# Optimization experiments

Hardware: AMD Instinct MI355X
Metric: run time of the kernel (lower is better)

Reference implementation:

```python
import jax, jax.numpy as jnp
import numpy as np

R, C, N, E, H, F, ED, G, L = 1, 4, 50000, 200000, 128, 128, 16, 64, 2


def setup_inputs() -> dict:
    key = jax.random.key(0)
    ks = jax.random.split(key, 16)
    s = 0.05
    return {
        "x": jax.random.normal(ks[0], (R * C * N, H), jnp.float32),
        "batch": jnp.sort(jax.random.randint(ks[1], (N,), 0, G)),
        "edge_index": jax.random.randint(ks[2], (2, E), 0, N),
        "edge_attr": jax.random.normal(ks[3], (1, 1, E, ED), jnp.float32),
        "node_mask": jax.random.uniform(ks[4], (R, C, N, 1), jnp.float32),
        "edge_mask": jax.random.uniform(ks[5], (R, C, E, 1), jnp.float32),
        "W_be": jax.random.normal(ks[6], (ED, H), jnp.float32) * s,
        "b_be": jnp.zeros((H,), jnp.float32),
        "eps": jnp.zeros((L,), jnp.float32),
        "W1": jax.random.normal(ks[7], (L, H, H), jnp.float32) * s,
        "b1": jnp.zeros((L, H), jnp.float32),
        "W2": jax.random.normal(ks[8], (L, H, H), jnp.float32) * s,
        "b2": jnp.zeros((L, H), jnp.float32),
        "Wm1": jax.random.normal(ks[9], (H, H), jnp.float32) * s,
        "bm1": jnp.zeros((H,), jnp.float32),
        "Wm2": jax.random.normal(ks[10], (H, F), jnp.float32) * s,
        "bm2": jnp.zeros((F,), jnp.float32),
    }


def reference(x, batch, edge_index, edge_attr, node_mask, edge_mask,
              W_be, b_be, eps, W1, b1, W2, b2, Wm1, bm1, Wm2, bm2):
    gelu = lambda v: jax.nn.gelu(v, approximate=False)  # torch F.gelu default is erf
    src, dst = edge_index[0], edge_index[1]
    # bond encoder, shared across conv layers: (1,1,E,H)
    ee = edge_attr @ W_be + b_be
    for l in range(L):
        ux = x.reshape(R, C, N, H)
        # gather + add + GELU + edge-weight multiply: (R,C,E,H)
        msg = gelu(ux[:, :, src, :] + ee) * edge_mask
        # scatter_sum over edges into destination nodes
        agg = jnp.zeros_like(ux).at[:, :, dst, :].add(msg)
        h = (1.0 + eps[l]) * x + agg.reshape(x.shape)
        # conv MLP: Linear -> GELU -> Linear, then outer GELU (norm=Identity, dropout=0)
        h = gelu(h @ W1[l] + b1[l]) @ W2[l] + b2[l]
        x = gelu(h)
    # final node MLP (PyG MLP, norm=None): Linear -> GELU -> Linear
    x = gelu(x @ Wm1 + bm1) @ Wm2 + bm2  # (R*C*N, F)
    x4 = x.reshape(R, C, N, F)
    # masked mean-pool per (repeat, centroid, graph)
    num = jnp.zeros((R, C, G, F), x.dtype).at[:, :, batch, :].add(x4 * node_mask)
    den = jnp.zeros((R, C, G, 1), x.dtype).at[:, :, batch, :].add(node_mask) + 1e-7
    pooled = (num / den).transpose(0, 2, 1, 3).reshape(-1, F)  # (R*G*C, F)
    return pooled
```

## Files before the change

### kernel.cpp

```cpp
#include <hip/hip_runtime.h>
#include <math.h>

#define NN 50000
#define EN 200000
#define CC 4
#define HH 128
#define GG 64
#define LDSA 136
#define LDSF 132

typedef __attribute__((ext_vector_type(8))) short bs8;
typedef __attribute__((ext_vector_type(4))) float f32x4;

__device__ __forceinline__ unsigned short f2bf(float f) {
  unsigned int u = __float_as_uint(f);
  u += 0x7FFFu + ((u >> 16) & 1u);
  return (unsigned short)(u >> 16);
}
__device__ __forceinline__ float bf2f(unsigned short h) {
  return __uint_as_float(((unsigned int)h) << 16);
}
__device__ __forceinline__ float gelu_f(float x) {
  float z = fabsf(x) * 0.7071067811865476f;
  float t = __builtin_amdgcn_rcpf(fmaf(0.3275911f, z, 1.0f));
  float poly = t * fmaf(t, fmaf(t, fmaf(t, fmaf(t, 1.061405429f, -1.453152027f),
                                        1.421413741f), -0.284496736f), 0.254829592f);
  float e = fmaf(-poly, __expf(-z * z), 1.0f);
  return 0.5f * x * (1.0f + copysignf(e, x));
}

__global__ __launch_bounds__(256) void count_kernel(const int* __restrict__ dst,
                                                    int* __restrict__ counts) {
  int e = blockIdx.x * 256 + threadIdx.x;
  if (e < EN) atomicAdd(&counts[dst[e]], 1);
}

__global__ __launch_bounds__(256) void block_sum_kernel(const int* __restrict__ counts,
                                                        int* __restrict__ bsums) {
  int tid = threadIdx.x;
  int i = blockIdx.x * 256 + tid;
  int v = (i < NN) ? counts[i] : 0;
#pragma unroll
  for (int d = 1; d < 64; d <<= 1) v += __shfl_xor(v, d);
  __shared__ int ws4[4];
  if ((tid & 63) == 0) ws4[tid >> 6] = v;
  __syncthreads();
  if (tid == 0) bsums[blockIdx.x] = ws4[0] + ws4[1] + ws4[2] + ws4[3];
}

__global__ __launch_bounds__(256) void bsum_scan_kernel(const int* __restrict__ bsums,
                                                        int* __restrict__ boffs, int nb) {
  int tid = threadIdx.x, lane = tid & 63, wv = tid >> 6;
  int v = (tid < nb) ? bsums[tid] : 0;
  int s = v;
#pragma unroll
  for (int d = 1; d < 64; d <<= 1) { int t = __shfl_up(s, d); if (lane >= d) s += t; }
  __shared__ int wsum[4];
  if (lane == 63) wsum[wv] = s;
  __syncthreads();
  int pre = 0;
  for (int j = 0; j < wv; ++j) pre += wsum[j];
  if (tid < nb) boffs[tid] = pre + s - v;
}

__global__ __launch_bounds__(256) void block_scan_kernel(const int* __restrict__ counts,
                                                         const int* __restrict__ boffs,
                                                         int* __restrict__ offsets,
                                                         int* __restrict__ cursor) {
  int tid = threadIdx.x, lane = tid & 63, wv = tid >> 6;
  int i = blockIdx.x * 256 + tid;
  int v = (i < NN) ? counts[i] : 0;
  int s = v;
#pragma unroll
  for (int d = 1; d < 64; d <<= 1) { int t = __shfl_up(s, d); if (lane >= d) s += t; }
  __shared__ int wsum[4];
  if (lane == 63) wsum[wv] = s;
  __syncthreads();
  int pre = boffs[blockIdx.x];
  for (int j = 0; j < wv; ++j) pre += wsum[j];
  if (i < NN) { int e = pre + s - v; offsets[i] = e; cursor[i] = e; }
  if (i == 0) offsets[NN] = EN;
}

__global__ __launch_bounds__(256) void fill_kernel(const int* __restrict__ dst,
                                                   int* __restrict__ cursor,
                                                   int* __restrict__ csr_e) {
  int e = blockIdx.x * 256 + threadIdx.x;
  if (e < EN) {
    int pos = atomicAdd(&cursor[dst[e]], 1);
    csr_e[pos] = e;
  }
}

__global__ __launch_bounds__(256) void prep_w_kernel(const float* __restrict__ W1,
                                                     const float* __restrict__ W2,
                                                     const float* __restrict__ Wm1,
                                                     const float* __restrict__ Wm2,
                                                     unsigned short* __restrict__ wts) {
  int m = blockIdx.x >> 6;
  int idx = (blockIdx.x & 63) * 256 + threadIdx.x;
  const float* src = (m == 0) ? W1 : (m == 1) ? W1 + 16384 : (m == 2) ? W2
                     : (m == 3) ? W2 + 16384 : (m == 4) ? Wm1 : Wm2;
  unsigned short* dhi = wts + m * 32768;
  unsigned short* dlo = dhi + 16384;
  int n = idx >> 7, k = idx & 127;
  float v = src[k * HH + n];
  unsigned short hi = f2bf(v);
  dhi[n * HH + k] = hi;
  dlo[n * HH + k] = f2bf(v - bf2f(hi));
}

__global__ __launch_bounds__(256) void ee_kernel(const float* __restrict__ eattr,
                                                 const float* __restrict__ Wbe,
                                                 const float* __restrict__ bbe,
                                                 float* __restrict__ ee) {
  __shared__ float Ws[16 * HH];
  __shared__ float Ea[16 * 16];
  int tid = threadIdx.x;
  int e0 = blockIdx.x * 16;
#pragma unroll
  for (int i = 0; i < 8; ++i) Ws[tid + i * 256] = Wbe[tid + i * 256];
  Ea[tid] = eattr[(size_t)e0 * 16 + tid];
  __syncthreads();
  int h = tid & 127, half = tid >> 7;
  float bb = bbe[h];
#pragma unroll
  for (int j = 0; j < 8; ++j) {
    int el = j * 2 + half;
    float acc = bb;
#pragma unroll
    for (int d = 0; d < 16; ++d) acc += Ea[el * 16 + d] * Ws[d * HH + h];
    ee[(size_t)(e0 + el) * HH + h] = acc;
  }
}

__global__ __launch_bounds__(256) void agg_kernel(const float* __restrict__ x,
                                                  const float* __restrict__ ee,
                                                  const float* __restrict__ emask,
                                                  const int* __restrict__ src,
                                                  const int* __restrict__ off,
                                                  const int* __restrict__ csr_e,
                                                  const float* __restrict__ epsp, int layer,
                                                  float* __restrict__ hout) {
  int wv = threadIdx.x >> 6, lane = threadIdx.x & 63;
  int v = blockIdx.x * 4 + wv;
  int h2 = lane * 2;
  float2 acc[CC];
#pragma unroll
  for (int c = 0; c < CC; ++c) { acc[c].x = 0.f; acc[c].y = 0.f; }
  int beg = off[v], end = off[v + 1];
  int e = 0, s = 0;
  if (beg < end) { e = csr_e[beg]; s = src[e]; }
  for (int t = beg; t < end; ++t) {
    int tn = t + 1;
    int e2 = 0, s2 = 0;
    if (tn < end) { e2 = csr_e[tn]; s2 = src[e2]; }
    float2 ev = *(const float2*)(ee + (size_t)e * HH + h2);
#pragma unroll
    for (int c = 0; c < CC; ++c) {
      float em = emask[c * EN + e];
      float2 xv = *(const float2*)(x + (size_t)(c * NN + s) * HH + h2);
      acc[c].x += gelu_f(xv.x + ev.x) * em;
      acc[c].y += gelu_f(xv.y + ev.y) * em;
    }
    e = e2; s = s2;
  }
  float ep = 1.0f + epsp[layer];
#pragma unroll
  for (int c = 0; c < CC; ++c) {
    float2 xs = *(const float2*)(x + (size_t)(c * NN + v) * HH + h2);
    float2 o;
    o.x = ep * xs.x + acc[c].x;
    o.y = ep * xs.y + acc[c].y;
    *(float2*)(hout + (size_t)(c * NN + v) * HH + h2) = o;
  }
}

__global__ __launch_bounds__(256, 2) void mlp_kernel(
    const float* __restrict__ in,
    const unsigned short* __restrict__ w1hi, const unsigned short* __restrict__ w1lo,
    const float* __restrict__ b1,
    const unsigned short* __restrict__ w2hi, const unsigned short* __restrict__ w2lo,
    const float* __restrict__ b2,
    float* __restrict__ out,
    const float* __restrict__ nmask, const int* __restrict__ batch,
    float* __restrict__ num, int mode) {
  __shared__ __align__(16) unsigned short AB[128 * LDSA];
  __shared__ int kk[64];
  unsigned short* Ahi = AB;
  unsigned short* Alo = AB + 64 * LDSA;
  int tid = threadIdx.x;
  int row0 = blockIdx.x * 64;
  int lane = tid & 63, wq = tid >> 6;
  int ln = lane & 15, quad = lane >> 4;

  bs8 b1h[4][2], b1l[4][2];
#pragma unroll
  for (int ks = 0; ks < 4; ++ks)
#pragma unroll
    for (int nt = 0; nt < 2; ++nt) {
      int wrow = ((wq * 2 + nt) * 16 + ln) * HH + ks * 32 + quad * 8;
      b1h[ks][nt] = *(const bs8*)(w1hi + wrow);
      b1l[ks][nt] = *(const bs8*)(w1lo + wrow);
    }

#pragma unroll
  for (int i = 0; i < 8; ++i) {
    int idx = tid + i * 256;
    int r = idx >> 5, c4 = idx & 31;
    float4 vv = *(const float4*)(in + (size_t)(row0 + r) * HH + c4 * 4);
    unsigned short h0 = f2bf(vv.x), h1 = f2bf(vv.y), h2 = f2bf(vv.z), h3 = f2bf(vv.w);
    ushort4 hv; hv.x = h0; hv.y = h1; hv.z = h2; hv.w = h3;
    ushort4 lv;
    lv.x = f2bf(vv.x - bf2f(h0)); lv.y = f2bf(vv.y - bf2f(h1));
    lv.z = f2bf(vv.z - bf2f(h2)); lv.w = f2bf(vv.w - bf2f(h3));
    *(ushort4*)(Ahi + r * LDSA + c4 * 4) = hv;
    *(ushort4*)(Alo + r * LDSA + c4 * 4) = lv;
  }
  __syncthreads();

  f32x4 acc[4][2];
#pragma unroll
  for (int mt = 0; mt < 4; ++mt)
#pragma unroll
    for (int nt = 0; nt < 2; ++nt)
#pragma unroll
      for (int r = 0; r < 4; ++r) acc[mt][nt][r] = 0.f;
#pragma unroll
  for (int ks = 0; ks < 4; ++ks) {
    bs8 ah[4], al[4];
#pragma unroll
    for (int mt = 0; mt < 4; ++mt) {
      ah[mt] = *(const bs8*)(Ahi + (mt * 16 + ln) * LDSA + ks * 32 + quad * 8);
      al[mt] = *(const bs8*)(Alo + (mt * 16 + ln) * LDSA + ks * 32 + quad * 8);
    }
#pragma unroll
    for (int nt = 0; nt < 2; ++nt)
#pragma unroll
      for (int mt = 0; mt < 4; ++mt) {
        acc[mt][nt] = __builtin_amdgcn_mfma_f32_16x16x32_bf16(al[mt], b1h[ks][nt], acc[mt][nt], 0, 0, 0);
        acc[mt][nt] = __builtin_amdgcn_mfma_f32_16x16x32_bf16(ah[mt], b1l[ks][nt], acc[mt][nt], 0, 0, 0);
        acc[mt][nt] = __builtin_amdgcn_mfma_f32_16x16x32_bf16(ah[mt], b1h[ks][nt], acc[mt][nt], 0, 0, 0);
      }
  }
  __syncthreads();

  bs8 b2h[4][2], b2l[4][2];
#pragma unroll
  for (int ks = 0; ks < 4; ++ks)
#pragma unroll
    for (int nt = 0; nt < 2; ++nt) {
      int wrow = ((wq * 2 + nt) * 16 + ln) * HH + ks * 32 + quad * 8;
      b2h[ks][nt] = *(const bs8*)(w2hi + wrow);
      b2l[ks][nt] = *(const bs8*)(w2lo + wrow);
    }

#pragma unroll
  for (int nt = 0; nt < 2; ++nt) {
    int col = (wq * 2 + nt) * 16 + ln;
    float bb = b1[col];
#pragma unroll
    for (int mt = 0; mt < 4; ++mt)
#pragma unroll
      for (int r = 0; r < 4; ++r) {
        float tv = gelu_f(acc[mt][nt][r] + bb);
        unsigned short th = f2bf(tv);
        int rr = mt * 16 + quad * 4 + r;
        Ahi[rr * LDSA + col] = th;
        Alo[rr * LDSA + col] = f2bf(tv - bf2f(th));
      }
  }
  __syncthreads();

#pragma unroll
  for (int mt = 0; mt < 4; ++mt)
#pragma unroll
    for (int nt = 0; nt < 2; ++nt)
#pragma unroll
      for (int r = 0; r < 4; ++r) acc[mt][nt][r] = 0.f;
  if (mode == 0) {
#pragma unroll
    for (int ks = 0; ks < 4; ++ks) {
      bs8 ah[4], al[4];
#pragma unroll
      for (int mt = 0; mt < 4; ++mt) {
        ah[mt] = *(const bs8*)(Ahi + (mt * 16 + ln) * LDSA + ks * 32 + quad * 8);
        al[mt] = *(const bs8*)(Alo + (mt * 16 + ln) * LDSA + ks * 32 + quad * 8);
      }
#pragma unroll
      for (int nt = 0; nt < 2; ++nt)
#pragma unroll
        for (int mt = 0; mt < 4; ++mt) {
          acc[mt][nt] = __builtin_amdgcn_mfma_f32_16x16x32_bf16(al[mt], b2h[ks][nt], acc[mt][nt], 0, 0, 0);
          acc[mt][nt] = __builtin_amdgcn_mfma_f32_16x16x32_bf16(ah[mt], b2l[ks][nt], acc[mt][nt], 0, 0, 0);
          acc[mt][nt] = __builtin_amdgcn_mfma_f32_16x16x32_bf16(ah[mt], b2h[ks][nt], acc[mt][nt], 0, 0, 0);
        }
    }
#pragma unroll
    for (int nt = 0; nt < 2; ++nt) {
      int col = (wq * 2 + nt) * 16 + ln;
      float bb = b2[col];
#pragma unroll
      for (int mt = 0; mt < 4; ++mt)
#pragma unroll
        for (int r = 0; r < 4; ++r) {
          float o = gelu_f(acc[mt][nt][r] + bb);
          out[(size_t)(row0 + mt * 16 + quad * 4 + r) * HH + col] = o;
        }
    }
  } else {
#pragma unroll
    for (int ks = 0; ks < 4; ++ks) {
      bs8 ah[4], al[4];
#pragma unroll
      for (int mt = 0; mt < 4; ++mt) {
        ah[mt] = *(const bs8*)(Ahi + (mt * 16 + ln) * LDSA + ks * 32 + quad * 8);
        al[mt] = *(const bs8*)(Alo + (mt * 16 + ln) * LDSA + ks * 32 + quad * 8);
      }
#pragma unroll
      for (int nt = 0; nt < 2; ++nt)
#pragma unroll
        for (int mt = 0; mt < 4; ++mt) {
          acc[mt][nt] = __builtin_amdgcn_mfma_f32_16x16x32_bf16(al[mt], b2h[ks][nt], acc[mt][nt], 0, 0, 0);
          acc[mt][nt] = __builtin_amdgcn_mfma_f32_16x16x32_bf16(ah[mt], b2l[ks][nt], acc[mt][nt], 0, 0, 0);
          acc[mt][nt] = __builtin_amdgcn_mfma_f32_16x16x32_bf16(ah[mt], b2h[ks][nt], acc[mt][nt], 0, 0, 0);
        }
    }
    __syncthreads();
    float* Tf = (float*)AB;
#pragma unroll
    for (int nt = 0; nt < 2; ++nt) {
      int col = (wq * 2 + nt) * 16 + ln;
      float bb = b2[col];
#pragma unroll
      for (int mt = 0; mt < 4; ++mt)
#pragma unroll
        for (int r = 0; r < 4; ++r) {
          int rl = mt * 16 + quad * 4 + r;
          int gr = row0 + rl;
          Tf[rl * LDSF + col] = (acc[mt][nt][r] + bb) * nmask[gr];
        }
    }
    if (tid < 64) {
      int gr = row0 + tid;
      int c = gr / NN;
      int n = gr - c * NN;
      kk[tid] = (c << 6) | batch[n];
    }
    __syncthreads();
    if (tid < 128) {
      int col = tid;
      float a2 = 0.f;
      int cur = kk[0];
      for (int r = 0; r < 64; ++r) {
        int k2 = kk[r];
        if (k2 != cur) {
          atomicAdd(&num[((size_t)(cur & 63) * CC + (cur >> 6)) * HH + col], a2);
          a2 = 0.f;
          cur = k2;
        }
        a2 += Tf[r * LDSF + col];
      }
      atomicAdd(&num[((size_t)(cur & 63) * CC + (cur >> 6)) * HH + col], a2);
    }
  }
}

__global__ __launch_bounds__(256) void pool_finalize_kernel(const float* __restrict__ num,
                                                            const int* __restrict__ batch,
                                                            const float* __restrict__ nmask,
                                                            float* __restrict__ outp) {
  int g = blockIdx.x >> 2, c = blockIdx.x & 3;
  int lo = 0, hi = NN;
  while (lo < hi) { int m = (lo + hi) >> 1; if (batch[m] < g) lo = m + 1; else hi = m; }
  int start = lo;
  hi = NN;
  while (lo < hi) { int m = (lo + hi) >> 1; if (batch[m] < g + 1) lo = m + 1; else hi = m; }
  int end = lo;
  int tid = threadIdx.x;
  float d = 0.f;
  for (int n = start + tid; n < end; n += 256) d += nmask[c * NN + n];
#pragma unroll
  for (int k = 1; k < 64; k <<= 1) d += __shfl_xor(d, k);
  __shared__ float ws4[4];
  if ((tid & 63) == 0) ws4[tid >> 6] = d;
  __syncthreads();
  float den = ws4[0] + ws4[1] + ws4[2] + ws4[3] + 1e-7f;
  if (tid < 128) {
    int idx = blockIdx.x * 128 + tid;
    outp[idx] = num[idx] / den;
  }
}

extern "C" void kernel_launch(void* const* d_in, const int* in_sizes, int n_in,
                              void* d_out, int out_size, void* d_ws, size_t ws_size,
                              hipStream_t stream) {
  const float* x_in  = (const float*)d_in[0];
  const int*   batch = (const int*)d_in[1];
  const int*   eidx  = (const int*)d_in[2];
  const float* eattr = (const float*)d_in[3];
  const float* nmask = (const float*)d_in[4];
  const float* emask = (const float*)d_in[5];
  const float* Wbe   = (const float*)d_in[6];
  const float* bbe   = (const float*)d_in[7];
  const float* epsp  = (const float*)d_in[8];
  const float* W1    = (const float*)d_in[9];
  const float* b1    = (const float*)d_in[10];
  const float* W2    = (const float*)d_in[11];
  const float* b2    = (const float*)d_in[12];
  const float* Wm1   = (const float*)d_in[13];
  const float* bm1   = (const float*)d_in[14];
  const float* Wm2   = (const float*)d_in[15];
  const float* bm2   = (const float*)d_in[16];
  float* outp = (float*)d_out;

  const int* srcp = eidx;
  const int* dstp = eidx + EN;

  char* ws = (char*)d_ws;
  float* ee   = (float*)(ws);
  float* hbuf = (float*)(ws + 102400000);
  float* xbuf = (float*)(ws + 204800000);
  int* counts  = (int*)(ws + 307200000);
  int* offsets = counts + NN;
  int* cursor  = offsets + NN + 1;
  int* csr_e   = cursor + NN;
  unsigned short* wts = (unsigned short*)(ws + 307200000 + 1400016);
  int* bsums = (int*)ws;
  int* boffs = (int*)(ws + 1024);
  float* num = (float*)ws;

  const int NB = (NN + 255) / 256;

  hipMemsetAsync(counts, 0, NN * sizeof(int), stream);
  count_kernel<<<(EN + 255) / 256, 256, 0, stream>>>(dstp, counts);
  block_sum_kernel<<<NB, 256, 0, stream>>>(counts, bsums);
  bsum_scan_kernel<<<1, 256, 0, stream>>>(bsums, boffs, NB);
  block_scan_kernel<<<NB, 256, 0, stream>>>(counts, boffs, offsets, cursor);
  fill_kernel<<<(EN + 255) / 256, 256, 0, stream>>>(dstp, cursor, csr_e);

  prep_w_kernel<<<384, 256, 0, stream>>>(W1, W2, Wm1, Wm2, wts);

  ee_kernel<<<EN / 16, 256, 0, stream>>>(eattr, Wbe, bbe, ee);

  agg_kernel<<<NN / 4, 256, 0, stream>>>(x_in, ee, emask, srcp, offsets, csr_e, epsp, 0, hbuf);
  mlp_kernel<<<(CC * NN) / 64, 256, 0, stream>>>(hbuf, wts + 0, wts + 16384, b1,
                                                 wts + 65536, wts + 81920, b2,
                                                 xbuf, nmask, batch, num, 0);
  agg_kernel<<<NN / 4, 256, 0, stream>>>(xbuf, ee, emask, srcp, offsets, csr_e, epsp, 1, hbuf);
  mlp_kernel<<<(CC * NN) / 64, 256, 0, stream>>>(hbuf, wts + 32768, wts + 49152, b1 + 128,
                                                 wts + 98304, wts + 114688, b2 + 128,
                                                 xbuf, nmask, batch, num, 0);
  hipMemsetAsync(num, 0, 131072, stream);
  mlp_kernel<<<(CC * NN) / 64, 256, 0, stream>>>(xbuf, wts + 131072, wts + 147456, bm1,
                                                 wts + 163840, wts + 180224, bm2,
                                                 (float*)nullptr, nmask, batch, num, 1);
  pool_finalize_kernel<<<GG * CC, 256, 0, stream>>>(num, batch, nmask, outp);
}
```

Baseline: 770.9 us.

## Fuse edge aggregation into per-layer MLP kernel with node-major activation layout

Merges the gather/GELU/scatter aggregation and the two-linear MLP into one layer kernel. Each block aggregates 16 nodes across all 4 centroids, with half-waves splitting edges and combining through shuffles, and writes the result straight into LDS as bf16 hi/lo tiles, so the fp32 hbuf round trip to global memory is gone. Intermediate activations move to a node-major (node, centroid) layout, so one gathered source node reads 4 contiguous rows, and the final MLP+pool kernel is adapted to that layout. The cost is that edge-gather latency now sits inside an MFMA kernel limited to 2 blocks per CU, and per-node degree imbalance stalls the whole block.

```diff
diff --git a/kernel.cpp b/kernel.cpp
--- a/kernel.cpp
+++ b/kernel.cpp
@@ -134,65 +134,28 @@
   }
 }
 
-__global__ __launch_bounds__(256) void agg_kernel(const float* __restrict__ x,
-                                                  const float* __restrict__ ee,
-                                                  const float* __restrict__ emask,
-                                                  const int* __restrict__ src,
-                                                  const int* __restrict__ off,
-                                                  const int* __restrict__ csr_e,
-                                                  const float* __restrict__ epsp, int layer,
-                                                  float* __restrict__ hout) {
-  int wv = threadIdx.x >> 6, lane = threadIdx.x & 63;
-  int v = blockIdx.x * 4 + wv;
-  int h2 = lane * 2;
-  float2 acc[CC];
-#pragma unroll
-  for (int c = 0; c < CC; ++c) { acc[c].x = 0.f; acc[c].y = 0.f; }
-  int beg = off[v], end = off[v + 1];
-  int e = 0, s = 0;
-  if (beg < end) { e = csr_e[beg]; s = src[e]; }
-  for (int t = beg; t < end; ++t) {
-    int tn = t + 1;
-    int e2 = 0, s2 = 0;
-    if (tn < end) { e2 = csr_e[tn]; s2 = src[e2]; }
-    float2 ev = *(const float2*)(ee + (size_t)e * HH + h2);
-#pragma unroll
-    for (int c = 0; c < CC; ++c) {
-      float em = emask[c * EN + e];
-      float2 xv = *(const float2*)(x + (size_t)(c * NN + s) * HH + h2);
-      acc[c].x += gelu_f(xv.x + ev.x) * em;
-      acc[c].y += gelu_f(xv.y + ev.y) * em;
-    }
-    e = e2; s = s2;
-  }
-  float ep = 1.0f + epsp[layer];
-#pragma unroll
-  for (int c = 0; c < CC; ++c) {
-    float2 xs = *(const float2*)(x + (size_t)(c * NN + v) * HH + h2);
-    float2 o;
-    o.x = ep * xs.x + acc[c].x;
-    o.y = ep * xs.y + acc[c].y;
-    *(float2*)(hout + (size_t)(c * NN + v) * HH + h2) = o;
-  }
-}
-
-__global__ __launch_bounds__(256, 2) void mlp_kernel(
-    const float* __restrict__ in,
+__global__ __launch_bounds__(256, 2) void layer_kernel(
+    const float* __restrict__ x, const float* __restrict__ ee,
+    const float* __restrict__ emask,
+    const int* __restrict__ src, const int* __restrict__ off,
+    const int* __restrict__ csr_e,
+    const float* __restrict__ epsp, int layer,
     const unsigned short* __restrict__ w1hi, const unsigned short* __restrict__ w1lo,
     const float* __restrict__ b1,
     const unsigned short* __restrict__ w2hi, const unsigned short* __restrict__ w2lo,
     const float* __restrict__ b2,
-    float* __restrict__ out,
-    const float* __restrict__ nmask, const int* __restrict__ batch,
-    float* __restrict__ num, int mode) {
+    float* __restrict__ out) {
   __shared__ __align__(16) unsigned short AB[128 * LDSA];
-  __shared__ int kk[64];
   unsigned short* Ahi = AB;
   unsigned short* Alo = AB + 64 * LDSA;
   int tid = threadIdx.x;
+  int lane = tid & 63, wv = tid >> 6;
+  int node0 = blockIdx.x * 16;
   int row0 = blockIdx.x * 64;
-  int lane = tid & 63, wq = tid >> 6;
+  int half = lane >> 5, l32 = lane & 31;
+  int c4 = l32 * 4;
   int ln = lane & 15, quad = lane >> 4;
+  int wq = wv;
 
   bs8 b1h[4][2], b1l[4][2];
 #pragma unroll
@@ -204,18 +167,59 @@
       b1l[ks][nt] = *(const bs8*)(w1lo + wrow);
     }
 
-#pragma unroll
-  for (int i = 0; i < 8; ++i) {
-    int idx = tid + i * 256;
-    int r = idx >> 5, c4 = idx & 31;
-    float4 vv = *(const float4*)(in + (size_t)(row0 + r) * HH + c4 * 4);
-    unsigned short h0 = f2bf(vv.x), h1 = f2bf(vv.y), h2 = f2bf(vv.z), h3 = f2bf(vv.w);
-    ushort4 hv; hv.x = h0; hv.y = h1; hv.z = h2; hv.w = h3;
-    ushort4 lv;
-    lv.x = f2bf(vv.x - bf2f(h0)); lv.y = f2bf(vv.y - bf2f(h1));
-    lv.z = f2bf(vv.z - bf2f(h2)); lv.w = f2bf(vv.w - bf2f(h3));
-    *(ushort4*)(Ahi + r * LDSA + c4 * 4) = hv;
-    *(ushort4*)(Alo + r * LDSA + c4 * 4) = lv;
+  float ep = 1.0f + epsp[layer];
+#pragma unroll
+  for (int j = 0; j < 4; ++j) {
+    int v = node0 + wv * 4 + j;
+    float4 acc[CC];
+#pragma unroll
+    for (int c = 0; c < CC; ++c) { acc[c].x = 0.f; acc[c].y = 0.f; acc[c].z = 0.f; acc[c].w = 0.f; }
+    int beg = off[v], end = off[v + 1];
+    int t0 = beg + half;
+    int e = 0, s = 0;
+    if (t0 < end) { e = csr_e[t0]; s = src[e]; }
+    for (int t = t0; t < end; t += 2) {
+      int tn = t + 2;
+      int e2 = 0, s2 = 0;
+      if (tn < end) { e2 = csr_e[tn]; s2 = src[e2]; }
+      float4 ev = *(const float4*)(ee + (size_t)e * HH + c4);
+#pragma unroll
+      for (int c = 0; c < CC; ++c) {
+        float em = emask[c * EN + e];
+        size_t xrow = (layer == 0) ? ((size_t)c * NN + s) : ((size_t)s * CC + c);
+        float4 xv = *(const float4*)(x + xrow * HH + c4);
+        acc[c].x += gelu_f(xv.x + ev.x) * em;
+        acc[c].y += gelu_f(xv.y + ev.y) * em;
+        acc[c].z += gelu_f(xv.z + ev.z) * em;
+        acc[c].w += gelu_f(xv.w + ev.w) * em;
+      }
+      e = e2; s = s2;
+    }
+#pragma unroll
+    for (int c = 0; c < CC; ++c) {
+      acc[c].x += __shfl_xor(acc[c].x, 32);
+      acc[c].y += __shfl_xor(acc[c].y, 32);
+      acc[c].z += __shfl_xor(acc[c].z, 32);
+      acc[c].w += __shfl_xor(acc[c].w, 32);
+    }
+#pragma unroll
+    for (int cc = 0; cc < 2; ++cc) {
+      int c = half * 2 + cc;
+      size_t srow = (layer == 0) ? ((size_t)c * NN + v) : ((size_t)v * CC + c);
+      float4 xs = *(const float4*)(x + srow * HH + c4);
+      float ox = fmaf(ep, xs.x, acc[c].x);
+      float oy = fmaf(ep, xs.y, acc[c].y);
+      float oz = fmaf(ep, xs.z, acc[c].z);
+      float ow = fmaf(ep, xs.w, acc[c].w);
+      unsigned short h0 = f2bf(ox), h1 = f2bf(oy), h2 = f2bf(oz), h3 = f2bf(ow);
+      ushort4 hv; hv.x = h0; hv.y = h1; hv.z = h2; hv.w = h3;
+      ushort4 lv;
+      lv.x = f2bf(ox - bf2f(h0)); lv.y = f2bf(oy - bf2f(h1));
+      lv.z = f2bf(oz - bf2f(h2)); lv.w = f2bf(ow - bf2f(h3));
+      int rl = (wv * 4 + j) * 4 + c;
+      *(ushort4*)(Ahi + rl * LDSA + c4) = hv;
+      *(ushort4*)(Alo + rl * LDSA + c4) = lv;
+    }
   }
   __syncthreads();
 
@@ -278,90 +282,187 @@
     for (int nt = 0; nt < 2; ++nt)
 #pragma unroll
       for (int r = 0; r < 4; ++r) acc[mt][nt][r] = 0.f;
-  if (mode == 0) {
-#pragma unroll
-    for (int ks = 0; ks < 4; ++ks) {
-      bs8 ah[4], al[4];
+#pragma unroll
+  for (int ks = 0; ks < 4; ++ks) {
+    bs8 ah[4], al[4];
+#pragma unroll
+    for (int mt = 0; mt < 4; ++mt) {
+      ah[mt] = *(const bs8*)(Ahi + (mt * 16 + ln) * LDSA + ks * 32 + quad * 8);
+      al[mt] = *(const bs8*)(Alo + (mt * 16 + ln) * LDSA + ks * 32 + quad * 8);
+    }
+#pragma unroll
+    for (int nt = 0; nt < 2; ++nt)
 #pragma unroll
       for (int mt = 0; mt < 4; ++mt) {
-        ah[mt] = *(const bs8*)(Ahi + (mt * 16 + ln) * LDSA + ks * 32 + quad * 8);
-        al[mt] = *(const bs8*)(Alo + (mt * 16 + ln) * LDSA + ks * 32 + quad * 8);
-      }
-#pragma unroll
-      for (int nt = 0; nt < 2; ++nt)
-#pragma unroll
-        for (int mt = 0; mt < 4; ++mt) {
-          acc[mt][nt] = __builtin_amdgcn_mfma_f32_16x16x32_bf16(al[mt], b2h[ks][nt], acc[mt][nt], 0, 0, 0);
-          acc[mt][nt] = __builtin_amdgcn_mfma_f32_16x16x32_bf16(ah[mt], b2l[ks][nt], acc[mt][nt], 0, 0, 0);
-          acc[mt][nt] = __builtin_amdgcn_mfma_f32_16x16x32_bf16(ah[mt], b2h[ks][nt], acc[mt][nt], 0, 0, 0);
-        }
-    }
+        acc[mt][nt] = __builtin_amdgcn_mfma_f32_16x16x32_bf16(al[mt], b2h[ks][nt], acc[mt][nt], 0, 0, 0);
+        acc[mt][nt] = __builtin_amdgcn_mfma_f32_16x16x32_bf16(ah[mt], b2l[ks][nt], acc[mt][nt], 0, 0, 0);
+        acc[mt][nt] = __builtin_amdgcn_mfma_f32_16x16x32_bf16(ah[mt], b2h[ks][nt], acc[mt][nt], 0, 0, 0);
+      }
+  }
+#pragma unroll
+  for (int nt = 0; nt < 2; ++nt) {
+    int col = (wq * 2 + nt) * 16 + ln;
+    float bb = b2[col];
+#pragma unroll
+    for (int mt = 0; mt < 4; ++mt)
+#pragma unroll
+      for (int r = 0; r < 4; ++r) {
+        float o = gelu_f(acc[mt][nt][r] + bb);
+        out[(size_t)(row0 + mt * 16 + quad * 4 + r) * HH + col] = o;
+      }
+  }
+}
+
+__global__ __launch_bounds__(256, 2) void mlp_pool_kernel(
+    const float* __restrict__ in,
+    const unsigned short* __restrict__ w1hi, const unsigned short* __restrict__ w1lo,
+    const float* __restrict__ b1,
+    const unsigned short* __restrict__ w2hi, const unsigned short* __restrict__ w2lo,
+    const float* __restrict__ b2,
+    const float* __restrict__ nmask, const int* __restrict__ batch,
+    float* __restrict__ num) {
+  __shared__ __align__(16) unsigned short AB[128 * LDSA];
+  __shared__ int kk[16];
+  unsigned short* Ahi = AB;
+  unsigned short* Alo = AB + 64 * LDSA;
+  int tid = threadIdx.x;
+  int row0 = blockIdx.x * 64;
+  int node0 = row0 >> 2;
+  int lane = tid & 63, wq = tid >> 6;
+  int ln = lane & 15, quad = lane >> 4;
+
+  bs8 b1h[4][2], b1l[4][2];
+#pragma unroll
+  for (int ks = 0; ks < 4; ++ks)
 #pragma unroll
     for (int nt = 0; nt < 2; ++nt) {
-      int col = (wq * 2 + nt) * 16 + ln;
-      float bb = b2[col];
-#pragma unroll
-      for (int mt = 0; mt < 4; ++mt)
-#pragma unroll
-        for (int r = 0; r < 4; ++r) {
-          float o = gelu_f(acc[mt][nt][r] + bb);
-          out[(size_t)(row0 + mt * 16 + quad * 4 + r) * HH + col] = o;
-        }
-    }
-  } else {
-#pragma unroll
-    for (int ks = 0; ks < 4; ++ks) {
-      bs8 ah[4], al[4];
+      int wrow = ((wq * 2 + nt) * 16 + ln) * HH + ks * 32 + quad * 8;
+      b1h[ks][nt] = *(const bs8*)(w1hi + wrow);
+      b1l[ks][nt] = *(const bs8*)(w1lo + wrow);
+    }
+#pragma unroll
+  for (int i = 0; i < 8; ++i) {
+    int idx = tid + i * 256;
+    int r = idx >> 5, cc4 = idx & 31;
+    float4 vv = *(const float4*)(in + (size_t)(row0 + r) * HH + cc4 * 4);
+    unsigned short h0 = f2bf(vv.x), h1 = f2bf(vv.y), h2 = f2bf(vv.z), h3 = f2bf(vv.w);
+    ushort4 hv; hv.x = h0; hv.y = h1; hv.z = h2; hv.w = h3;
+    ushort4 lv;
+    lv.x = f2bf(vv.x - bf2f(h0)); lv.y = f2bf(vv.y - bf2f(h1));
+    lv.z = f2bf(vv.z - bf2f(h2)); lv.w = f2bf(vv.w - bf2f(h3));
+    *(ushort4*)(Ahi + r * LDSA + cc4 * 4) = hv;
+    *(ushort4*)(Alo + r * LDSA + cc4 * 4) = lv;
+  }
+  if (tid < 16) kk[tid] = batch[node0 + tid];
+  __syncthreads();
+
+  f32x4 acc[4][2];
+#pragma unroll
+  for (int mt = 0; mt < 4; ++mt)
+#pragma unroll
+    for (int nt = 0; nt < 2; ++nt)
+#pragma unroll
+      for (int r = 0; r < 4; ++r) acc[mt][nt][r] = 0.f;
+#pragma unroll
+  for (int ks = 0; ks < 4; ++ks) {
+    bs8 ah[4], al[4];
+#pragma unroll
+    for (int mt = 0; mt < 4; ++mt) {
+      ah[mt] = *(const bs8*)(Ahi + (mt * 16 + ln) * LDSA + ks * 32 + quad * 8);
+      al[mt] = *(const bs8*)(Alo + (mt * 16 + ln) * LDSA + ks * 32 + quad * 8);
+    }
+#pragma unroll
+    for (int nt = 0; nt < 2; ++nt)
 #pragma unroll
       for (int mt = 0; mt < 4; ++mt) {
-        ah[mt] = *(const bs8*)(Ahi + (mt * 16 + ln) * LDSA + ks * 32 + quad * 8);
-        al[mt] = *(const bs8*)(Alo + (mt * 16 + ln) * LDSA + ks * 32 + quad * 8);
-      }
-#pragma unroll
-      for (int nt = 0; nt < 2; ++nt)
-#pragma unroll
-        for (int mt = 0; mt < 4; ++mt) {
-          acc[mt][nt] = __builtin_amdgcn_mfma_f32_16x16x32_bf16(al[mt], b2h[ks][nt], acc[mt][nt], 0, 0, 0);
-          acc[mt][nt] = __builtin_amdgcn_mfma_f32_16x16x32_bf16(ah[mt], b2l[ks][nt], acc[mt][nt], 0, 0, 0);
-          acc[mt][nt] = __builtin_amdgcn_mfma_f32_16x16x32_bf16(ah[mt], b2h[ks][nt], acc[mt][nt], 0, 0, 0);
-        }
-    }
-    __syncthreads();
-    float* Tf = (float*)AB;
+        acc[mt][nt] = __builtin_amdgcn_mfma_f32_16x16x32_bf16(al[mt], b1h[ks][nt], acc[mt][nt], 0, 0, 0);
+        acc[mt][nt] = __builtin_amdgcn_mfma_f32_16x16x32_bf16(ah[mt], b1l[ks][nt], acc[mt][nt], 0, 0, 0);
+        acc[mt][nt] = __builtin_amdgcn_mfma_f32_16x16x32_bf16(ah[mt], b1h[ks][nt], acc[mt][nt], 0, 0, 0);
+      }
+  }
+  __syncthreads();
+
+  bs8 b2h[4][2], b2l[4][2];
+#pragma unroll
+  for (int ks = 0; ks < 4; ++ks)
 #pragma unroll
     for (int nt = 0; nt < 2; ++nt) {
-      int col = (wq * 2 + nt) * 16 + ln;
-      float bb = b2[col];
-#pragma unroll
-      for (int mt = 0; mt < 4; ++mt)
-#pragma unroll
-        for (int r = 0; r < 4; ++r) {
-          int rl = mt * 16 + quad * 4 + r;
-          int gr = row0 + rl;
-          Tf[rl * LDSF + col] = (acc[mt][nt][r] + bb) * nmask[gr];
-        }
-    }
-    if (tid < 64) {
-      int gr = row0 + tid;
-      int c = gr / NN;
-      int n = gr - c * NN;
-      kk[tid] = (c << 6) | batch[n];
-    }
-    __syncthreads();
-    if (tid < 128) {
-      int col = tid;
+      int wrow = ((wq * 2 + nt) * 16 + ln) * HH + ks * 32 + quad * 8;
+      b2h[ks][nt] = *(const bs8*)(w2hi + wrow);
+      b2l[ks][nt] = *(const bs8*)(w2lo + wrow);
+    }
+#pragma unroll
+  for (int nt = 0; nt < 2; ++nt) {
+    int col = (wq * 2 + nt) * 16 + ln;
+    float bb = b1[col];
+#pragma unroll
+    for (int mt = 0; mt < 4; ++mt)
+#pragma unroll
+      for (int r = 0; r < 4; ++r) {
+        float tv = gelu_f(acc[mt][nt][r] + bb);
+        unsigned short th = f2bf(tv);
+        int rr = mt * 16 + quad * 4 + r;
+        Ahi[rr * LDSA + col] = th;
+        Alo[rr * LDSA + col] = f2bf(tv - bf2f(th));
+      }
+  }
+  __syncthreads();
+
+#pragma unroll
+  for (int mt = 0; mt < 4; ++mt)
+#pragma unroll
+    for (int nt = 0; nt < 2; ++nt)
+#pragma unroll
+      for (int r = 0; r < 4; ++r) acc[mt][nt][r] = 0.f;
+#pragma unroll
+  for (int ks = 0; ks < 4; ++ks) {
+    bs8 ah[4], al[4];
+#pragma unroll
+    for (int mt = 0; mt < 4; ++mt) {
+      ah[mt] = *(const bs8*)(Ahi + (mt * 16 + ln) * LDSA + ks * 32 + quad * 8);
+      al[mt] = *(const bs8*)(Alo + (mt * 16 + ln) * LDSA + ks * 32 + quad * 8);
+    }
+#pragma unroll
+    for (int nt = 0; nt < 2; ++nt)
+#pragma unroll
+      for (int mt = 0; mt < 4; ++mt) {
+        acc[mt][nt] = __builtin_amdgcn_mfma_f32_16x16x32_bf16(al[mt], b2h[ks][nt], acc[mt][nt], 0, 0, 0);
+        acc[mt][nt] = __builtin_amdgcn_mfma_f32_16x16x32_bf16(ah[mt], b2l[ks][nt], acc[mt][nt], 0, 0, 0);
+        acc[mt][nt] = __builtin_amdgcn_mfma_f32_16x16x32_bf16(ah[mt], b2h[ks][nt], acc[mt][nt], 0, 0, 0);
+      }
+  }
+  __syncthreads();
+  float* Tf = (float*)AB;
+#pragma unroll
+  for (int nt = 0; nt < 2; ++nt) {
+    int col = (wq * 2 + nt) * 16 + ln;
+    float bb = b2[col];
+#pragma unroll
+    for (int mt = 0; mt < 4; ++mt)
+#pragma unroll
+      for (int r = 0; r < 4; ++r) {
+        int rl = mt * 16 + quad * 4 + r;
+        int n = node0 + (rl >> 2), c = rl & 3;
+        Tf[rl * LDSF + col] = (acc[mt][nt][r] + bb) * nmask[c * NN + n];
+      }
+  }
+  __syncthreads();
+  if (tid < 128) {
+    int col = tid;
+#pragma unroll
+    for (int c = 0; c < 4; ++c) {
       float a2 = 0.f;
       int cur = kk[0];
-      for (int r = 0; r < 64; ++r) {
-        int k2 = kk[r];
-        if (k2 != cur) {
-          atomicAdd(&num[((size_t)(cur & 63) * CC + (cur >> 6)) * HH + col], a2);
+      for (int nl = 0; nl < 16; ++nl) {
+        int g2 = kk[nl];
+        if (g2 != cur) {
+          atomicAdd(&num[((size_t)cur * CC + c) * HH + col], a2);
           a2 = 0.f;
-          cur = k2;
+          cur = g2;
         }
-        a2 += Tf[r * LDSF + col];
-      }
-      atomicAdd(&num[((size_t)(cur & 63) * CC + (cur >> 6)) * HH + col], a2);
+        a2 += Tf[(nl * 4 + c) * LDSF + col];
+      }
+      atomicAdd(&num[((size_t)cur * CC + c) * HH + col], a2);
     }
   }
 }
@@ -418,9 +519,9 @@
   const int* dstp = eidx + EN;
 
   char* ws = (char*)d_ws;
-  float* ee   = (float*)(ws);
-  float* hbuf = (float*)(ws + 102400000);
-  float* xbuf = (float*)(ws + 204800000);
+  float* ee = (float*)(ws);
+  float* x2 = (float*)(ws + 102400000);
+  float* x1 = (float*)(ws + 204800000);
   int* counts  = (int*)(ws + 307200000);
   int* offsets = counts + NN;
   int* cursor  = offsets + NN + 1;
@@ -443,17 +544,15 @@
 
   ee_kernel<<<EN / 16, 256, 0, stream>>>(eattr, Wbe, bbe, ee);
 
-  agg_kernel<<<NN / 4, 256, 0, stream>>>(x_in, ee, emask, srcp, offsets, csr_e, epsp, 0, hbuf);
-  mlp_kernel<<<(CC * NN) / 64, 256, 0, stream>>>(hbuf, wts + 0, wts + 16384, b1,
-                                                 wts + 65536, wts + 81920, b2,
-                                                 xbuf, nmask, batch, num, 0);
-  agg_kernel<<<NN / 4, 256, 0, stream>>>(xbuf, ee, emask, srcp, offsets, csr_e, epsp, 1, hbuf);
-  mlp_kernel<<<(CC * NN) / 64, 256, 0, stream>>>(hbuf, wts + 32768, wts + 49152, b1 + 128,
-                                                 wts + 98304, wts + 114688, b2 + 128,
-                                                 xbuf, nmask, batch, num, 0);
+  layer_kernel<<<NN / 16, 256, 0, stream>>>(x_in, ee, emask, srcp, offsets, csr_e, epsp, 0,
+                                            wts + 0, wts + 16384, b1,
+                                            wts + 65536, wts + 81920, b2, x1);
+  layer_kernel<<<NN / 16, 256, 0, stream>>>(x1, ee, emask, srcp, offsets, csr_e, epsp, 1,
+                                            wts + 32768, wts + 49152, b1 + 128,
+                                            wts + 98304, wts + 114688, b2 + 128, x2);
   hipMemsetAsync(num, 0, 131072, stream);
-  mlp_kernel<<<(CC * NN) / 64, 256, 0, stream>>>(xbuf, wts + 131072, wts + 147456, bm1,
-                                                 wts + 163840, wts + 180224, bm2,
-                                                 (float*)nullptr, nmask, batch, num, 1);
+  mlp_pool_kernel<<<(CC * NN) / 64, 256, 0, stream>>>(x2, wts + 131072, wts + 147456, bm1,
+                                                      wts + 163840, wts + 180224, bm2,
+                                                      nmask, batch, num);
   pool_finalize_kernel<<<GG * CC, 256, 0, stream>>>(num, batch, nmask, outp);
 }
```

Result: slower. 900.1 us (+16.8%).

## Split edge loop across half-waves in agg and use per-wave MLP kernel

Applied to the files above, without the earlier changes.

The aggregation kernel now has each half-wave process alternate edges using float4 loads, then combines the partial sums with a cross-half shuffle. Each half writes two of the four channel outputs. The layer MLPs use a new kernel where each wave owns 16 rows and keeps its A fragments in registers. Weights are streamed from global memory or cache instead of being held in registers, LDS is used only for the per-wave intermediate, and block barriers are removed. This trades more weight loads per MFMA for higher occupancy (3 blocks) and no syncthreads, and the pooling MLP is split into its own kernel.

```diff
diff --git a/kernel.cpp b/kernel.cpp
--- a/kernel.cpp
+++ b/kernel.cpp
@@ -144,47 +144,154 @@
                                                   float* __restrict__ hout) {
   int wv = threadIdx.x >> 6, lane = threadIdx.x & 63;
   int v = blockIdx.x * 4 + wv;
-  int h2 = lane * 2;
-  float2 acc[CC];
-#pragma unroll
-  for (int c = 0; c < CC; ++c) { acc[c].x = 0.f; acc[c].y = 0.f; }
+  int half = lane >> 5, l32 = lane & 31;
+  int c4 = l32 * 4;
+  float4 acc[CC];
+#pragma unroll
+  for (int c = 0; c < CC; ++c) { acc[c].x = 0.f; acc[c].y = 0.f; acc[c].z = 0.f; acc[c].w = 0.f; }
   int beg = off[v], end = off[v + 1];
+  int t0 = beg + half;
   int e = 0, s = 0;
-  if (beg < end) { e = csr_e[beg]; s = src[e]; }
-  for (int t = beg; t < end; ++t) {
-    int tn = t + 1;
+  if (t0 < end) { e = csr_e[t0]; s = src[e]; }
+  for (int t = t0; t < end; t += 2) {
+    int tn = t + 2;
     int e2 = 0, s2 = 0;
     if (tn < end) { e2 = csr_e[tn]; s2 = src[e2]; }
-    float2 ev = *(const float2*)(ee + (size_t)e * HH + h2);
+    float4 ev = *(const float4*)(ee + (size_t)e * HH + c4);
 #pragma unroll
     for (int c = 0; c < CC; ++c) {
       float em = emask[c * EN + e];
-      float2 xv = *(const float2*)(x + (size_t)(c * NN + s) * HH + h2);
+      float4 xv = *(const float4*)(x + ((size_t)c * NN + s) * HH + c4);
       acc[c].x += gelu_f(xv.x + ev.x) * em;
       acc[c].y += gelu_f(xv.y + ev.y) * em;
+      acc[c].z += gelu_f(xv.z + ev.z) * em;
+      acc[c].w += gelu_f(xv.w + ev.w) * em;
     }
     e = e2; s = s2;
   }
+#pragma unroll
+  for (int c = 0; c < CC; ++c) {
+    acc[c].x += __shfl_xor(acc[c].x, 32);
+    acc[c].y += __shfl_xor(acc[c].y, 32);
+    acc[c].z += __shfl_xor(acc[c].z, 32);
+    acc[c].w += __shfl_xor(acc[c].w, 32);
+  }
   float ep = 1.0f + epsp[layer];
 #pragma unroll
-  for (int c = 0; c < CC; ++c) {
-    float2 xs = *(const float2*)(x + (size_t)(c * NN + v) * HH + h2);
-    float2 o;
-    o.x = ep * xs.x + acc[c].x;
-    o.y = ep * xs.y + acc[c].y;
-    *(float2*)(hout + (size_t)(c * NN + v) * HH + h2) = o;
-  }
-}
-
-__global__ __launch_bounds__(256, 2) void mlp_kernel(
+  for (int cc = 0; cc < 2; ++cc) {
+    int c = half * 2 + cc;
+    float4 xs = *(const float4*)(x + ((size_t)c * NN + v) * HH + c4);
+    float4 o;
+    o.x = fmaf(ep, xs.x, acc[c].x);
+    o.y = fmaf(ep, xs.y, acc[c].y);
+    o.z = fmaf(ep, xs.z, acc[c].z);
+    o.w = fmaf(ep, xs.w, acc[c].w);
+    *(float4*)(hout + ((size_t)c * NN + v) * HH + c4) = o;
+  }
+}
+
+__global__ __launch_bounds__(256, 3) void mlp_fast_kernel(
     const float* __restrict__ in,
     const unsigned short* __restrict__ w1hi, const unsigned short* __restrict__ w1lo,
     const float* __restrict__ b1,
     const unsigned short* __restrict__ w2hi, const unsigned short* __restrict__ w2lo,
     const float* __restrict__ b2,
-    float* __restrict__ out,
+    float* __restrict__ out) {
+  __shared__ __align__(16) unsigned short T[4][2][16 * LDSA];
+  int tid = threadIdx.x;
+  int lane = tid & 63, wv = tid >> 6;
+  int ln = lane & 15, quad = lane >> 4;
+  int row0 = blockIdx.x * 64 + wv * 16;
+  unsigned short* Thi = &T[wv][0][0];
+  unsigned short* Tlo = &T[wv][1][0];
+
+  bs8 ahi[4], alo[4];
+#pragma unroll
+  for (int ks = 0; ks < 4; ++ks) {
+    const float* p = in + (size_t)(row0 + ln) * HH + ks * 32 + quad * 8;
+    float4 v0 = *(const float4*)p;
+    float4 v1 = *(const float4*)(p + 4);
+    bs8 h, l;
+    h[0] = f2bf(v0.x); h[1] = f2bf(v0.y); h[2] = f2bf(v0.z); h[3] = f2bf(v0.w);
+    h[4] = f2bf(v1.x); h[5] = f2bf(v1.y); h[6] = f2bf(v1.z); h[7] = f2bf(v1.w);
+    l[0] = f2bf(v0.x - bf2f(h[0])); l[1] = f2bf(v0.y - bf2f(h[1]));
+    l[2] = f2bf(v0.z - bf2f(h[2])); l[3] = f2bf(v0.w - bf2f(h[3]));
+    l[4] = f2bf(v1.x - bf2f(h[4])); l[5] = f2bf(v1.y - bf2f(h[5]));
+    l[6] = f2bf(v1.z - bf2f(h[6])); l[7] = f2bf(v1.w - bf2f(h[7]));
+    ahi[ks] = h; alo[ks] = l;
+  }
+
+  f32x4 acc[8];
+#pragma unroll
+  for (int nt = 0; nt < 8; ++nt)
+#pragma unroll
+    for (int r = 0; r < 4; ++r) acc[nt][r] = 0.f;
+#pragma unroll
+  for (int nt = 0; nt < 8; ++nt)
+#pragma unroll
+    for (int ks = 0; ks < 4; ++ks) {
+      int wrow = (nt * 16 + ln) * HH + ks * 32 + quad * 8;
+      bs8 bh = *(const bs8*)(w1hi + wrow);
+      bs8 bl = *(const bs8*)(w1lo + wrow);
+      acc[nt] = __builtin_amdgcn_mfma_f32_16x16x32_bf16(alo[ks], bh, acc[nt], 0, 0, 0);
+      acc[nt] = __builtin_amdgcn_mfma_f32_16x16x32_bf16(ahi[ks], bl, acc[nt], 0, 0, 0);
+      acc[nt] = __builtin_amdgcn_mfma_f32_16x16x32_bf16(ahi[ks], bh, acc[nt], 0, 0, 0);
+    }
+
+#pragma unroll
+  for (int nt = 0; nt < 8; ++nt) {
+    int col = nt * 16 + ln;
+    float bb = b1[col];
+#pragma unroll
+    for (int r = 0; r < 4; ++r) {
+      float tv = gelu_f(acc[nt][r] + bb);
+      unsigned short th = f2bf(tv);
+      int rr = quad * 4 + r;
+      Thi[rr * LDSA + col] = th;
+      Tlo[rr * LDSA + col] = f2bf(tv - bf2f(th));
+    }
+  }
+#pragma unroll
+  for (int ks = 0; ks < 4; ++ks) {
+    ahi[ks] = *(const bs8*)(Thi + ln * LDSA + ks * 32 + quad * 8);
+    alo[ks] = *(const bs8*)(Tlo + ln * LDSA + ks * 32 + quad * 8);
+  }
+
+#pragma unroll
+  for (int nt = 0; nt < 8; ++nt)
+#pragma unroll
+    for (int r = 0; r < 4; ++r) acc[nt][r] = 0.f;
+#pragma unroll
+  for (int nt = 0; nt < 8; ++nt)
+#pragma unroll
+    for (int ks = 0; ks < 4; ++ks) {
+      int wrow = (nt * 16 + ln) * HH + ks * 32 + quad * 8;
+      bs8 bh = *(const bs8*)(w2hi + wrow);
+      bs8 bl = *(const bs8*)(w2lo + wrow);
+      acc[nt] = __builtin_amdgcn_mfma_f32_16x16x32_bf16(alo[ks], bh, acc[nt], 0, 0, 0);
+      acc[nt] = __builtin_amdgcn_mfma_f32_16x16x32_bf16(ahi[ks], bl, acc[nt], 0, 0, 0);
+      acc[nt] = __builtin_amdgcn_mfma_f32_16x16x32_bf16(ahi[ks], bh, acc[nt], 0, 0, 0);
+    }
+#pragma unroll
+  for (int nt = 0; nt < 8; ++nt) {
+    int col = nt * 16 + ln;
+    float bb = b2[col];
+#pragma unroll
+    for (int r = 0; r < 4; ++r) {
+      float o = gelu_f(acc[nt][r] + bb);
+      out[(size_t)(row0 + quad * 4 + r) * HH + col] = o;
+    }
+  }
+}
+
+__global__ __launch_bounds__(256, 2) void mlp_pool_kernel(
+    const float* __restrict__ in,
+    const unsigned short* __restrict__ w1hi, const unsigned short* __restrict__ w1lo,
+    const float* __restrict__ b1,
+    const unsigned short* __restrict__ w2hi, const unsigned short* __restrict__ w2lo,
+    const float* __restrict__ b2,
     const float* __restrict__ nmask, const int* __restrict__ batch,
-    float* __restrict__ num, int mode) {
+    float* __restrict__ num) {
   __shared__ __align__(16) unsigned short AB[128 * LDSA];
   __shared__ int kk[64];
   unsigned short* Ahi = AB;
@@ -203,19 +310,24 @@
       b1h[ks][nt] = *(const bs8*)(w1hi + wrow);
       b1l[ks][nt] = *(const bs8*)(w1lo + wrow);
     }
-
 #pragma unroll
   for (int i = 0; i < 8; ++i) {
     int idx = tid + i * 256;
-    int r = idx >> 5, c4 = idx & 31;
-    float4 vv = *(const float4*)(in + (size_t)(row0 + r) * HH + c4 * 4);
+    int r = idx >> 5, cc4 = idx & 31;
+    float4 vv = *(const float4*)(in + (size_t)(row0 + r) * HH + cc4 * 4);
     unsigned short h0 = f2bf(vv.x), h1 = f2bf(vv.y), h2 = f2bf(vv.z), h3 = f2bf(vv.w);
     ushort4 hv; hv.x = h0; hv.y = h1; hv.z = h2; hv.w = h3;
     ushort4 lv;
     lv.x = f2bf(vv.x - bf2f(h0)); lv.y = f2bf(vv.y - bf2f(h1));
     lv.z = f2bf(vv.z - bf2f(h2)); lv.w = f2bf(vv.w - bf2f(h3));
-    *(ushort4*)(Ahi + r * LDSA + c4 * 4) = hv;
-    *(ushort4*)(Alo + r * LDSA + c4 * 4) = lv;
+    *(ushort4*)(Ahi + r * LDSA + cc4 * 4) = hv;
+    *(ushort4*)(Alo + r * LDSA + cc4 * 4) = lv;
+  }
+  if (tid < 64) {
+    int gr = row0 + tid;
+    int c = gr / NN;
+    int n = gr - c * NN;
+    kk[tid] = (c << 6) | batch[n];
   }
   __syncthreads();
 
@@ -254,7 +366,6 @@
       b2h[ks][nt] = *(const bs8*)(w2hi + wrow);
       b2l[ks][nt] = *(const bs8*)(w2lo + wrow);
     }
-
 #pragma unroll
   for (int nt = 0; nt < 2; ++nt) {
     int col = (wq * 2 + nt) * 16 + ln;
@@ -278,91 +389,53 @@
     for (int nt = 0; nt < 2; ++nt)
 #pragma unroll
       for (int r = 0; r < 4; ++r) acc[mt][nt][r] = 0.f;
-  if (mode == 0) {
-#pragma unroll
-    for (int ks = 0; ks < 4; ++ks) {
-      bs8 ah[4], al[4];
+#pragma unroll
+  for (int ks = 0; ks < 4; ++ks) {
+    bs8 ah[4], al[4];
+#pragma unroll
+    for (int mt = 0; mt < 4; ++mt) {
+      ah[mt] = *(const bs8*)(Ahi + (mt * 16 + ln) * LDSA + ks * 32 + quad * 8);
+      al[mt] = *(const bs8*)(Alo + (mt * 16 + ln) * LDSA + ks * 32 + quad * 8);
+    }
+#pragma unroll
+    for (int nt = 0; nt < 2; ++nt)
 #pragma unroll
       for (int mt = 0; mt < 4; ++mt) {
-        ah[mt] = *(const bs8*)(Ahi + (mt * 16 + ln) * LDSA + ks * 32 + quad * 8);
-        al[mt] = *(const bs8*)(Alo + (mt * 16 + ln) * LDSA + ks * 32 + quad * 8);
+        acc[mt][nt] = __builtin_amdgcn_mfma_f32_16x16x32_bf16(al[mt], b2h[ks][nt], acc[mt][nt], 0, 0, 0);
+        acc[mt][nt] = __builtin_amdgcn_mfma_f32_16x16x32_bf16(ah[mt], b2l[ks][nt], acc[mt][nt], 0, 0, 0);
+        acc[mt][nt] = __builtin_amdgcn_mfma_f32_16x16x32_bf16(ah[mt], b2h[ks][nt], acc[mt][nt], 0, 0, 0);
       }
-#pragma unroll
-      for (int nt = 0; nt < 2; ++nt)
-#pragma unroll
-        for (int mt = 0; mt < 4; ++mt) {
-          acc[mt][nt] = __builtin_amdgcn_mfma_f32_16x16x32_bf16(al[mt], b2h[ks][nt], acc[mt][nt], 0, 0, 0);
-          acc[mt][nt] = __builtin_amdgcn_mfma_f32_16x16x32_bf16(ah[mt], b2l[ks][nt], acc[mt][nt], 0, 0, 0);
-          acc[mt][nt] = __builtin_amdgcn_mfma_f32_16x16x32_bf16(ah[mt], b2h[ks][nt], acc[mt][nt], 0, 0, 0);
-        }
-    }
-#pragma unroll
-    for (int nt = 0; nt < 2; ++nt) {
-      int col = (wq * 2 + nt) * 16 + ln;
-      float bb = b2[col];
-#pragma unroll
-      for (int mt = 0; mt < 4; ++mt)
-#pragma unroll
-        for (int r = 0; r < 4; ++r) {
-          float o = gelu_f(acc[mt][nt][r] + bb);
-          out[(size_t)(row0 + mt * 16 + quad * 4 + r) * HH + col] = o;
-        }
-    }
-  } else {
-#pragma unroll
-    for (int ks = 0; ks < 4; ++ks) {
-      bs8 ah[4], al[4];
-#pragma unroll
-      for (int mt = 0; mt < 4; ++mt) {
-        ah[mt] = *(const bs8*)(Ahi + (mt * 16 + ln) * LDSA + ks * 32 + quad * 8);
-        al[mt] = *(const bs8*)(Alo + (mt * 16 + ln) * LDSA + ks * 32 + quad * 8);
+  }
+  __syncthreads();
+  float* Tf = (float*)AB;
+#pragma unroll
+  for (int nt = 0; nt < 2; ++nt) {
+    int col = (wq * 2 + nt) * 16 + ln;
+    float bb = b2[col];
+#pragma unroll
+    for (int mt = 0; mt < 4; ++mt)
+#pragma unroll
+      for (int r = 0; r < 4; ++r) {
+        int rl = mt * 16 + quad * 4 + r;
+        int gr = row0 + rl;
+        Tf[rl * LDSF + col] = (acc[mt][nt][r] + bb) * nmask[gr];
       }
-#pragma unroll
-      for (int nt = 0; nt < 2; ++nt)
-#pragma unroll
-        for (int mt = 0; mt < 4; ++mt) {
-          acc[mt][nt] = __builtin_amdgcn_mfma_f32_16x16x32_bf16(al[mt], b2h[ks][nt], acc[mt][nt], 0, 0, 0);
-          acc[mt][nt] = __builtin_amdgcn_mfma_f32_16x16x32_bf16(ah[mt], b2l[ks][nt], acc[mt][nt], 0, 0, 0);
-          acc[mt][nt] = __builtin_amdgcn_mfma_f32_16x16x32_bf16(ah[mt], b2h[ks][nt], acc[mt][nt], 0, 0, 0);
-        }
-    }
-    __syncthreads();
-    float* Tf = (float*)AB;
-#pragma unroll
-    for (int nt = 0; nt < 2; ++nt) {
-      int col = (wq * 2 + nt) * 16 + ln;
-      float bb = b2[col];
-#pragma unroll
-      for (int mt = 0; mt < 4; ++mt)
-#pragma unroll
-        for (int r = 0; r < 4; ++r) {
-          int rl = mt * 16 + quad * 4 + r;
-          int gr = row0 + rl;
-          Tf[rl * LDSF + col] = (acc[mt][nt][r] + bb) * nmask[gr];
-        }
-    }
-    if (tid < 64) {
-      int gr = row0 + tid;
-      int c = gr / NN;
-      int n = gr - c * NN;
-      kk[tid] = (c << 6) | batch[n];
-    }
-    __syncthreads();
-    if (tid < 128) {
-      int col = tid;
-      float a2 = 0.f;
-      int cur = kk[0];
-      for (int r = 0; r < 64; ++r) {
-        int k2 = kk[r];
-        if (k2 != cur) {
-          atomicAdd(&num[((size_t)(cur & 63) * CC + (cur >> 6)) * HH + col], a2);
-          a2 = 0.f;
-          cur = k2;
-        }
-        a2 += Tf[r * LDSF + col];
+  }
+  __syncthreads();
+  if (tid < 128) {
+    int col = tid;
+    float a2 = 0.f;
+    int cur = kk[0];
+    for (int r = 0; r < 64; ++r) {
+      int k2 = kk[r];
+      if (k2 != cur) {
+        atomicAdd(&num[((size_t)(cur & 63) * CC + (cur >> 6)) * HH + col], a2);
+        a2 = 0.f;
+        cur = k2;
       }
-      atomicAdd(&num[((size_t)(cur & 63) * CC + (cur >> 6)) * HH + col], a2);
-    }
+      a2 += Tf[r * LDSF + col];
+    }
+    atomicAdd(&num[((size_t)(cur & 63) * CC + (cur >> 6)) * HH + col], a2);
   }
 }
 
@@ -444,16 +517,14 @@
   ee_kernel<<<EN / 16, 256, 0, stream>>>(eattr, Wbe, bbe, ee);
 
   agg_kernel<<<NN / 4, 256, 0, stream>>>(x_in, ee, emask, srcp, offsets, csr_e, epsp, 0, hbuf);
-  mlp_kernel<<<(CC * NN) / 64, 256, 0, stream>>>(hbuf, wts + 0, wts + 16384, b1,
-                                                 wts + 65536, wts + 81920, b2,
-                                                 xbuf, nmask, batch, num, 0);
+  mlp_fast_kernel<<<(CC * NN) / 64, 256, 0, stream>>>(hbuf, wts + 0, wts + 16384, b1,
+                                                      wts + 65536, wts + 81920, b2, xbuf);
   agg_kernel<<<NN / 4, 256, 0, stream>>>(xbuf, ee, emask, srcp, offsets, csr_e, epsp, 1, hbuf);
-  mlp_kernel<<<(CC * NN) / 64, 256, 0, stream>>>(hbuf, wts + 32768, wts + 49152, b1 + 128,
-                                                 wts + 98304, wts + 114688, b2 + 128,
-                                                 xbuf, nmask, batch, num, 0);
+  mlp_fast_kernel<<<(CC * NN) / 64, 256, 0, stream>>>(hbuf, wts + 32768, wts + 49152, b1 + 128,
+                                                      wts + 98304, wts + 114688, b2 + 128, xbuf);
   hipMemsetAsync(num, 0, 131072, stream);
-  mlp_kernel<<<(CC * NN) / 64, 256, 0, stream>>>(xbuf, wts + 131072, wts + 147456, bm1,
-                                                 wts + 163840, wts + 180224, bm2,
-                                                 (float*)nullptr, nmask, batch, num, 1);
+  mlp_pool_kernel<<<(CC * NN) / 64, 256, 0, stream>>>(xbuf, wts + 131072, wts + 147456, bm1,
+                                                      wts + 163840, wts + 180224, bm2,
+                                                      nmask, batch, num);
   pool_finalize_kernel<<<GG * CC, 256, 0, stream>>>(num, batch, nmask, outp);
 }
```

Result: slower. 982.7 us (+27.5%).
